# Performance work log

Measured on AMD Instinct MI355X. Metric: run time of the kernel, lower is better.

Reference implementation:

```python
import jax, jax.numpy as jnp
import numpy as np

N = 65536      # total nodes (cells) in batch
E = 262144     # edges per edge type
T = 3          # edge types: row, col, diag
D = 128        # hidden_dim
HG = 4         # gat_heads
DHG = D // HG  # 32, GAT head dim
HH = 4         # hgt_heads
DHH = D // HH  # 32, HGT head dim
B = 32         # boards per batch
SLOPE = 0.2
EPS = 1e-6


def setup_inputs():
    ks = jax.random.split(jax.random.key(0), 32)
    def nrm(i, shape, s=0.05):
        return (jax.random.normal(ks[i], shape) * s).astype(jnp.float32)
    inp = {
        'x_cell': nrm(0, (N, D), 1.0),
        'z_h': nrm(1, (B, D), 1.0),
        'x_cell_embedded': nrm(2, (N, D), 1.0),
        'edge_index': jax.random.randint(ks[3], (T, 2, E), 0, N, dtype=jnp.int32),
        'batch_size': B,
        # GAT conv 1 (one GATConv per edge type, summed)
        'gat1_W': nrm(4, (T, D, D), 0.09),
        'gat1_asrc': nrm(5, (T, HG, DHG), 0.12),
        'gat1_adst': nrm(6, (T, HG, DHG), 0.12),
        'gat1_b': jnp.zeros((T, D), jnp.float32),
        # GAT conv 2
        'gat2_W': nrm(7, (T, D, D), 0.09),
        'gat2_asrc': nrm(8, (T, HG, DHG), 0.12),
        'gat2_adst': nrm(9, (T, HG, DHG), 0.12),
        'gat2_b': jnp.zeros((T, D), jnp.float32),
        # RMSNorms
        'norm1_s': jnp.ones((D,), jnp.float32),
        'norm2_s': jnp.ones((D,), jnp.float32),
        'norm3_s': jnp.ones((D,), jnp.float32),
        # HGT (single node type 'cell', T edge types)
        'hgt_Wk': nrm(10, (D, D), 0.09), 'hgt_bk': jnp.zeros((D,), jnp.float32),
        'hgt_Wq': nrm(11, (D, D), 0.09), 'hgt_bq': jnp.zeros((D,), jnp.float32),
        'hgt_Wv': nrm(12, (D, D), 0.09), 'hgt_bv': jnp.zeros((D,), jnp.float32),
        'hgt_arel': nrm(13, (T, HH, DHH, DHH), 0.15),
        'hgt_mrel': nrm(14, (T, HH, DHH, DHH), 0.15),
        'hgt_prel': jnp.ones((T, HH), jnp.float32),
        'hgt_Wo': nrm(15, (D, D), 0.09), 'hgt_bo': jnp.zeros((D,), jnp.float32),
        'hgt_skip': jnp.ones((), jnp.float32),
        # input injection
        'inj_W': nrm(16, (D, D), 0.09), 'inj_b': jnp.zeros((D,), jnp.float32),
        # FiLM
        'film_W1': nrm(17, (D, 2 * D), 0.09), 'film_b1': jnp.zeros((2 * D,), jnp.float32),
        'film_W2': nrm(18, (2 * D, 2 * D), 0.001), 'film_b2': jnp.zeros((2 * D,), jnp.float32),
    }
    return inp


def _rmsnorm(x, scale):
    return scale * x * jax.lax.rsqrt(jnp.mean(x * x, axis=-1, keepdims=True) + EPS)


def _res(x_old, x_new, scale):
    return jax.nn.leaky_relu(x_old + _rmsnorm(x_new, scale), SLOPE)


def _gat_sum(x, W, asrc, adst, b, src, dst):
    """HeteroConv(sum) over T GATConvs (concat heads, add_self_loops)."""
    loop = jnp.arange(N, dtype=src.dtype)
    def one(Wt, a_s, a_d, bt, s, t):
        s = jnp.concatenate([s, loop])   # self loops
        t = jnp.concatenate([t, loop])
        h = (x @ Wt).reshape(N, HG, DHG)             # [N,H,Dh]
        alpha_src = (h * a_s).sum(-1)                # [N,H]
        alpha_dst = (h * a_d).sum(-1)
        e = jax.nn.leaky_relu(alpha_src[s] + alpha_dst[t], SLOPE)  # [E+N,H]
        m = jax.ops.segment_max(e, t, num_segments=N)
        ex = jnp.exp(e - m[t])
        denom = jax.ops.segment_sum(ex, t, num_segments=N)
        alpha = ex / (denom[t] + 1e-16)
        out = jax.ops.segment_sum(alpha[:, :, None] * h[s], t, num_segments=N)
        return out.reshape(N, D) + bt
    return jax.vmap(one)(W, asrc, adst, b, src, dst).sum(0)


def _hgt(x, Wk, bk, Wq, bq, Wv, bv, a_rel, m_rel, p_rel, Wo, bo, skip, src, dst):
    k = (x @ Wk + bk).reshape(N, HH, DHH)
    q = (x @ Wq + bq).reshape(N, HH, DHH)
    v = (x @ Wv + bv).reshape(N, HH, DHH)
    # per-edge-type relation transforms at node level, then gather per edge
    k_t = jnp.einsum('nhd,thdf->tnhf', k, a_rel)    # [T,N,H,Dk]
    v_t = jnp.einsum('nhd,thdf->tnhf', v, m_rel)
    k_e = jax.vmap(lambda a, i: a[i])(k_t, src)     # [T,E,H,Dk]
    v_e = jax.vmap(lambda a, i: a[i])(v_t, src)
    score = (q[dst] * k_e).sum(-1) * p_rel[:, None, :] / np.sqrt(DHH)  # [T,E,H]
    score = score.reshape(T * E, HH)
    dst_f = dst.reshape(-1)
    m = jax.ops.segment_max(score, dst_f, num_segments=N)
    ex = jnp.exp(score - m[dst_f])
    denom = jax.ops.segment_sum(ex, dst_f, num_segments=N)
    alpha = ex / (denom[dst_f] + 1e-16)
    agg = jax.ops.segment_sum(alpha[:, :, None] * v_e.reshape(T * E, HH, DHH),
                              dst_f, num_segments=N)          # [N,H,Dk]
    out = jax.nn.gelu(agg.reshape(N, D), approximate=False) @ Wo + bo
    sig = jax.nn.sigmoid(skip)
    return sig * out + (1.0 - sig) * x


def _film(nodes, z_h, W1, b1, W2, b2, bsz):
    gb = jax.nn.gelu(z_h @ W1 + b1, approximate=False) @ W2 + b2  # [B,2D]
    gamma, beta = jnp.split(gb, 2, axis=-1)
    gamma = 0.1 * jnp.tanh(gamma)
    beta = 0.1 * jnp.tanh(beta)
    c = N // bsz
    out = (1.0 + gamma)[:, None, :] * nodes.reshape(bsz, c, D) + beta[:, None, :]
    return out.reshape(N, D)


def reference(x_cell, z_h, x_cell_embedded,
              gat1_W, gat1_asrc, gat1_adst, gat1_b,
              gat2_W, gat2_asrc, gat2_adst, gat2_b,
              norm1_s, norm2_s, norm3_s,
              hgt_Wk, hgt_bk, hgt_Wq, hgt_bq, hgt_Wv, hgt_bv,
              hgt_arel, hgt_mrel, hgt_prel, hgt_Wo, hgt_bo, hgt_skip,
              inj_W, inj_b, film_W1, film_b1, film_W2, film_b2,
              edge_index, batch_size):
    src = edge_index[:, 0]
    dst = edge_index[:, 1]
    x1 = _res(x_cell, _gat_sum(x_cell, gat1_W, gat1_asrc, gat1_adst, gat1_b, src, dst), norm1_s)
    x2 = _res(x1, _gat_sum(x1, gat2_W, gat2_asrc, gat2_adst, gat2_b, src, dst), norm2_s)
    x3 = _res(x2, _hgt(x2, hgt_Wk, hgt_bk, hgt_Wq, hgt_bq, hgt_Wv, hgt_bv,
                       hgt_arel, hgt_mrel, hgt_prel, hgt_Wo, hgt_bo, hgt_skip,
                       src, dst), norm3_s)
    x3 = x3 + x_cell_embedded @ inj_W + inj_b
    return _film(x3, z_h, film_W1, film_b1, film_W2, film_b2, batch_size)
```

## Files before the change

### kernel.cpp

```cpp
#include <hip/hip_runtime.h>

#define NN 65536
#define EE 262144
#define ND ((size_t)NN * 128)
#define TBW 132

typedef unsigned short u16;
typedef short bf8_t __attribute__((ext_vector_type(8)));
typedef float f32x4 __attribute__((ext_vector_type(4)));

__device__ __forceinline__ float lrelu(float x){ return x > 0.f ? x : 0.2f*x; }
__device__ __forceinline__ float gelu_exact(float x){ return 0.5f*x*(1.f+erff(x*0.70710678118654752f)); }
__device__ __forceinline__ u16 f2bf(float f){
    union { float f; unsigned u; } v; v.f = f;
    unsigned u = v.u;
    return (u16)((u + 0x7FFFu + ((u >> 16) & 1u)) >> 16);
}
__device__ __forceinline__ float bf2f(u16 b){
    union { unsigned u; float f; } v; v.u = ((unsigned)b) << 16; return v.f;
}
__device__ __forceinline__ float2 bf2x(unsigned p){
    union { unsigned u; float f; } a, b;
    a.u = (p & 0xFFFFu) << 16; b.u = p & 0xFFFF0000u;
    return make_float2(a.f, b.f);
}
__device__ __forceinline__ unsigned cvt2(float a, float b){
    unsigned r; asm("v_cvt_pk_bf16_f32 %0, %1, %2" : "=v"(r) : "v"(a), "v"(b)); return r;
}

__device__ __forceinline__ void load_af32(const float* __restrict__ X, int row, int lk, bf8_t* af){
    #pragma unroll
    for (int kk = 0; kk < 4; ++kk){
        const float* p = X + (size_t)row*128 + kk*32 + lk*8;
        float4 a = *(const float4*)p;
        float4 b = *(const float4*)(p+4);
        union { bf8_t v; unsigned u[4]; } r;
        r.u[0] = cvt2(a.x, a.y); r.u[1] = cvt2(a.z, a.w);
        r.u[2] = cvt2(b.x, b.y); r.u[3] = cvt2(b.z, b.w);
        af[kk] = r.v;
    }
}
__device__ __forceinline__ void load_af16(const u16* __restrict__ X, int row, int lk, bf8_t* af){
    #pragma unroll
    for (int kk = 0; kk < 4; ++kk)
        af[kk] = *(const bf8_t*)(X + (size_t)row*128 + kk*32 + lk*8);
}
__device__ __forceinline__ void mfma_w1(const bf8_t* af, const u16* __restrict__ Wp,
                                        int lr, int lk, f32x4* acc){
    #pragma unroll
    for (int i = 0; i < 8; ++i) acc[i] = (f32x4){0.f,0.f,0.f,0.f};
    #pragma unroll
    for (int kk = 0; kk < 4; ++kk){
        bf8_t B[8];
        #pragma unroll
        for (int nt = 0; nt < 8; ++nt)
            B[nt] = *(const bf8_t*)&Wp[(nt*16+lr)*128 + kk*32 + lk*8];
        #pragma unroll
        for (int nt = 0; nt < 8; ++nt)
            acc[nt] = __builtin_amdgcn_mfma_f32_16x16x32_bf16(af[kk], B[nt], acc[nt], 0, 0, 0);
    }
}
__device__ __forceinline__ void mfma_w2(const bf8_t* af0, const bf8_t* af1,
                                        const u16* __restrict__ Wp,
                                        int lr, int lk, f32x4* acc0, f32x4* acc1){
    #pragma unroll
    for (int i = 0; i < 8; ++i){ acc0[i] = (f32x4){0.f,0.f,0.f,0.f}; acc1[i] = (f32x4){0.f,0.f,0.f,0.f}; }
    #pragma unroll
    for (int kk = 0; kk < 4; ++kk){
        bf8_t B[8];
        #pragma unroll
        for (int nt = 0; nt < 8; ++nt)
            B[nt] = *(const bf8_t*)&Wp[(nt*16+lr)*128 + kk*32 + lk*8];
        #pragma unroll
        for (int nt = 0; nt < 8; ++nt){
            acc0[nt] = __builtin_amdgcn_mfma_f32_16x16x32_bf16(af0[kk], B[nt], acc0[nt], 0, 0, 0);
            acc1[nt] = __builtin_amdgcn_mfma_f32_16x16x32_bf16(af1[kk], B[nt], acc1[nt], 0, 0, 0);
        }
    }
}
__device__ __forceinline__ void acc_to_tb(u16 (*tbw)[TBW], const f32x4* acc, int lr, int lk, const float* bias){
    asm volatile("s_waitcnt lgkmcnt(0)" ::: "memory");
    #pragma unroll
    for (int nt = 0; nt < 8; ++nt){
        int col = nt*16 + lr;
        float badd = bias ? bias[col] : 0.f;
        #pragma unroll
        for (int i = 0; i < 4; ++i) tbw[lk*4+i][col] = f2bf(acc[nt][i] + badd);
    }
    asm volatile("s_waitcnt lgkmcnt(0)" ::: "memory");
}
__device__ __forceinline__ void tb_store(const u16 (*tbw)[TBW], u16* __restrict__ O, int rowbase, int lr, int lk){
    #pragma unroll
    for (int c = 0; c < 4; ++c){
        bf8_t v = *(const bf8_t*)&tbw[c*4+lk][lr*8];
        *(bf8_t*)(O + (size_t)(rowbase + c*4 + lk)*128 + lr*8) = v;
    }
}
__device__ __forceinline__ void tb_frags(const u16 (*tbw)[TBW], int lr, int lk, bf8_t* ha){
    #pragma unroll
    for (int kk = 0; kk < 4; ++kk) ha[kk] = *(const bf8_t*)&tbw[lr][kk*32 + lk*8];
}

__global__ __launch_bounds__(256) void wpack_k(
    const float* __restrict__ g1W, const float* __restrict__ g2W,
    const float* __restrict__ Wk, const float* __restrict__ Wq, const float* __restrict__ Wv,
    const float* __restrict__ Wo, const float* __restrict__ injW,
    const float* __restrict__ arel, const float* __restrict__ mrel,
    const float* __restrict__ g1as, const float* __restrict__ g1ad,
    const float* __restrict__ g2as, const float* __restrict__ g2ad,
    u16* __restrict__ wp, u16* __restrict__ wpa)
{
    int b = blockIdx.x, tid = threadIdx.x;
    if (b < 17) {
        const float* src; int rel = 0;
        if (b < 3) src = g1W + b*16384;
        else if (b < 6) src = g2W + (b-3)*16384;
        else if (b == 6) src = Wk;
        else if (b == 7) src = Wq;
        else if (b == 8) src = Wv;
        else if (b == 9) src = Wo;
        else if (b == 10) src = injW;
        else if (b < 14) { src = arel + (b-11)*4096; rel = 1; }
        else { src = mrel + (b-14)*4096; rel = 1; }
        u16* dst = wp + (size_t)b*16384;
        for (int idx = tid; idx < 16384; idx += 256) {
            int n = idx >> 7, k = idx & 127;
            float v;
            if (rel) v = ((n>>5)==(k>>5)) ? src[(n>>5)*1024 + (k&31)*32 + (n&31)] : 0.f;
            else v = src[k*128 + n];
            dst[idx] = f2bf(v);
        }
    } else {
        for (int idx = tid; idx < 6*2048; idx += 256) {
            int m = idx >> 11;
            int j = idx & 2047;
            int cg = j >> 7, k = j & 127;
            const float* as = (m < 3) ? g1as : g2as;
            const float* ad = (m < 3) ? g1ad : g2ad;
            int t = (m < 3) ? m : m - 3;
            float v = 0.f;
            if (cg < 4)      { if ((k>>5)==cg)   v = as[t*128 + cg*32 + (k&31)]; }
            else if (cg < 8) { int g = cg-4; if ((k>>5)==g) v = ad[t*128 + g*32 + (k&31)]; }
            wpa[idx] = f2bf(v);
        }
    }
}

__global__ __launch_bounds__(256, 2) void gat_gemm3_k(const float* __restrict__ X,
    const u16* __restrict__ wpg, const u16* __restrict__ wpa,
    u16* __restrict__ hb, float* __restrict__ alsb, float* __restrict__ aldb)
{
    __shared__ u16 tb[4][16][TBW];
    const int tid = threadIdx.x, wave = tid>>6, lane = tid&63, lr = lane&15, lk = lane>>4;
    const int rw0 = blockIdx.x*128 + wave*32;
    bf8_t af0[4], af1[4];
    load_af32(X, rw0 + lr, lk, af0);
    load_af32(X, rw0 + 16 + lr, lk, af1);
    f32x4 acc0[8], acc1[8];
    for (int t = 0; t < 3; ++t) {
        mfma_w2(af0, af1, wpg + t*16384, lr, lk, acc0, acc1);
        bf8_t Ba[4];
        #pragma unroll
        for (int kk = 0; kk < 4; ++kk)
            Ba[kk] = *(const bf8_t*)&wpa[t*2048 + lr*128 + kk*32 + lk*8];
        u16* h = hb + (size_t)t*ND;
        float* alst = alsb + (size_t)t*NN*4;
        float* aldt = aldb + (size_t)t*NN*4;
        {
            acc_to_tb(tb[wave], acc0, lr, lk, nullptr);
            tb_store(tb[wave], h, rw0, lr, lk);
            bf8_t ha[4]; tb_frags(tb[wave], lr, lk, ha);
            f32x4 a2 = (f32x4){0.f,0.f,0.f,0.f};
            #pragma unroll
            for (int kk = 0; kk < 4; ++kk)
                a2 = __builtin_amdgcn_mfma_f32_16x16x32_bf16(ha[kk], Ba[kk], a2, 0, 0, 0);
            if (lr < 8){
                float* dp = (lr < 4) ? alst : aldt;
                int g = lr & 3;
                #pragma unroll
                for (int i = 0; i < 4; ++i) dp[(size_t)(rw0 + lk*4 + i)*4 + g] = a2[i];
            }
        }
        {
            acc_to_tb(tb[wave], acc1, lr, lk, nullptr);
            tb_store(tb[wave], h, rw0 + 16, lr, lk);
            bf8_t ha[4]; tb_frags(tb[wave], lr, lk, ha);
            f32x4 a2 = (f32x4){0.f,0.f,0.f,0.f};
            #pragma unroll
            for (int kk = 0; kk < 4; ++kk)
                a2 = __builtin_amdgcn_mfma_f32_16x16x32_bf16(ha[kk], Ba[kk], a2, 0, 0, 0);
            if (lr < 8){
                float* dp = (lr < 4) ? alst : aldt;
                int g = lr & 3;
                #pragma unroll
                for (int i = 0; i < 4; ++i) dp[(size_t)(rw0 + 16 + lk*4 + i)*4 + g] = a2[i];
            }
        }
    }
}

__global__ __launch_bounds__(256, 2) void hgt_proj_k(const float* __restrict__ X,
    const u16* __restrict__ wpk, const u16* __restrict__ wpq, const u16* __restrict__ wpv,
    const u16* __restrict__ wparel, const u16* __restrict__ wpmrel,
    const float* __restrict__ bk, const float* __restrict__ bq, const float* __restrict__ bv,
    u16* __restrict__ qb, u16* __restrict__ ktb, u16* __restrict__ vtb)
{
    __shared__ u16 tb[4][16][TBW];
    const int tid = threadIdx.x, wave = tid>>6, lane = tid&63, lr = lane&15, lk = lane>>4;
    const int rw0 = blockIdx.x*128 + wave*32;
    bf8_t af0[4], af1[4];
    load_af32(X, rw0 + lr, lk, af0);
    load_af32(X, rw0 + 16 + lr, lk, af1);
    f32x4 acc0[8], acc1[8];
    bf8_t ha0[4], ha1[4];
    mfma_w2(af0, af1, wpk, lr, lk, acc0, acc1);
    acc_to_tb(tb[wave], acc0, lr, lk, bk); tb_frags(tb[wave], lr, lk, ha0);
    acc_to_tb(tb[wave], acc1, lr, lk, bk); tb_frags(tb[wave], lr, lk, ha1);
    for (int t = 0; t < 3; ++t){
        mfma_w2(ha0, ha1, wparel + t*16384, lr, lk, acc0, acc1);
        u16* o = ktb + (size_t)t*ND;
        acc_to_tb(tb[wave], acc0, lr, lk, nullptr); tb_store(tb[wave], o, rw0, lr, lk);
        acc_to_tb(tb[wave], acc1, lr, lk, nullptr); tb_store(tb[wave], o, rw0 + 16, lr, lk);
    }
    mfma_w2(af0, af1, wpq, lr, lk, acc0, acc1);
    acc_to_tb(tb[wave], acc0, lr, lk, bq); tb_store(tb[wave], qb, rw0, lr, lk);
    acc_to_tb(tb[wave], acc1, lr, lk, bq); tb_store(tb[wave], qb, rw0 + 16, lr, lk);
    mfma_w2(af0, af1, wpv, lr, lk, acc0, acc1);
    acc_to_tb(tb[wave], acc0, lr, lk, bv); tb_frags(tb[wave], lr, lk, ha0);
    acc_to_tb(tb[wave], acc1, lr, lk, bv); tb_frags(tb[wave], lr, lk, ha1);
    for (int t = 0; t < 3; ++t){
        mfma_w2(ha0, ha1, wpmrel + t*16384, lr, lk, acc0, acc1);
        u16* o = vtb + (size_t)t*ND;
        acc_to_tb(tb[wave], acc0, lr, lk, nullptr); tb_store(tb[wave], o, rw0, lr, lk);
        acc_to_tb(tb[wave], acc1, lr, lk, nullptr); tb_store(tb[wave], o, rw0 + 16, lr, lk);
    }
}

__global__ __launch_bounds__(256) void final_k(const u16* __restrict__ aggb,
    const u16* __restrict__ wpo, const float* __restrict__ bo,
    const float* __restrict__ x2, const float* __restrict__ skipp, const float* __restrict__ scale,
    const float* __restrict__ xemb, const u16* __restrict__ wpinj, const float* __restrict__ injb,
    const float* __restrict__ gbuf, const int* __restrict__ bszp,
    float* __restrict__ out)
{
    const int tid = threadIdx.x, wave = tid>>6, lane = tid&63, lr = lane&15, lk = lane>>4;
    const int rw = blockIdx.x*64 + wave*16;
    bf8_t afa[4]; load_af16(aggb, rw + lr, lk, afa);
    f32x4 acc[8]; mfma_w1(afa, wpo, lr, lk, acc);
    const float sig = 1.f/(1.f + expf(-skipp[0]));
    float vv[8][4], xv[8][4], ss[4] = {0.f,0.f,0.f,0.f};
    #pragma unroll
    for (int nt = 0; nt < 8; ++nt){
        int col = nt*16 + lr;
        float badd = bo[col];
        #pragma unroll
        for (int i = 0; i < 4; ++i){
            float h = acc[nt][i] + badd;
            float x = x2[(size_t)(rw + lk*4 + i)*128 + col];
            float v = sig*h + (1.f - sig)*x;
            vv[nt][i] = v; xv[nt][i] = x;
            ss[i] += v*v;
        }
    }
    #pragma unroll
    for (int i = 0; i < 4; ++i){
        #pragma unroll
        for (int o = 1; o < 16; o <<= 1) ss[i] += __shfl_xor(ss[i], o);
    }
    float rr[4];
    #pragma unroll
    for (int i = 0; i < 4; ++i) rr[i] = rsqrtf(ss[i]*(1.f/128.f) + 1e-6f);
    #pragma unroll
    for (int nt = 0; nt < 8; ++nt){
        int col = nt*16 + lr;
        float sc = scale[col];
        #pragma unroll
        for (int i = 0; i < 4; ++i)
            vv[nt][i] = lrelu(xv[nt][i] + sc*vv[nt][i]*rr[i]);
    }
    bf8_t af2[4]; load_af32(xemb, rw + lr, lk, af2);
    f32x4 acc2[8]; mfma_w1(af2, wpinj, lr, lk, acc2);
    const int cpb = NN / *bszp;
    #pragma unroll
    for (int i = 0; i < 4; ++i){
        int row = rw + lk*4 + i;
        const float* gr = gbuf + (row / cpb)*256;
        #pragma unroll
        for (int nt = 0; nt < 8; ++nt){
            int col = nt*16 + lr;
            float h = vv[nt][i] + acc2[nt][i] + injb[col];
            out[(size_t)row*128 + col] = (1.f + gr[col])*h + gr[128 + col];
        }
    }
}

__global__ __launch_bounds__(256) void hist_k(const int* __restrict__ ei, int* __restrict__ cnt){
    int gid = blockIdx.x*256 + threadIdx.x;
    int t = gid / EE, e = gid - t*EE;
    int d = ei[t*2*EE + EE + e];
    atomicAdd(&cnt[t*NN + d], 1);
}
__global__ __launch_bounds__(256) void scan1_k(const int* __restrict__ cnt, int* __restrict__ off, int* __restrict__ parts){
    __shared__ int sums[256];
    int b = blockIdx.x; int t = b >> 6; int base = (b & 63) * 1024;
    int tid = threadIdx.x;
    int v[4]; int tsum = 0;
    int gbase = t*NN + base + tid*4;
    #pragma unroll
    for (int i = 0; i < 4; ++i){ v[i] = cnt[gbase+i]; tsum += v[i]; }
    sums[tid] = tsum; __syncthreads();
    for (int ofs = 1; ofs < 256; ofs <<= 1) {
        int a = (tid >= ofs) ? sums[tid-ofs] : 0;
        __syncthreads();
        sums[tid] += a;
        __syncthreads();
    }
    int run = sums[tid] - tsum;
    int obase = t*(NN+1) + base + tid*4;
    #pragma unroll
    for (int i = 0; i < 4; ++i){ off[obase+i] = run; run += v[i]; }
    if (tid == 255) parts[b] = sums[255];
}
__global__ void scan2_k(int* parts){
    if (threadIdx.x == 0 && blockIdx.x == 0) {
        for (int t = 0; t < 3; ++t) {
            int run = 0;
            for (int i = 0; i < 64; ++i) { int b = t*64+i; int v = parts[b]; parts[b] = run; run += v; }
        }
    }
}
__global__ __launch_bounds__(256) void scan3_k(int* __restrict__ off, const int* __restrict__ parts){
    int b = blockIdx.x; int t = b >> 6; int base = (b & 63) * 1024;
    int add = parts[b];
    int idx = t*(NN+1) + base + threadIdx.x*4;
    #pragma unroll
    for (int i = 0; i < 4; ++i) off[idx+i] += add;
    if (threadIdx.x == 0 && (b & 63) == 0) off[t*(NN+1) + NN] = EE;
}
__global__ __launch_bounds__(256) void scatter_k(const int* __restrict__ ei, const int* __restrict__ off,
                                                 int* __restrict__ cur, int* __restrict__ out){
    int gid = blockIdx.x*256 + threadIdx.x;
    int t = gid / EE, e = gid - t*EE;
    int s = ei[t*2*EE + e];
    int d = ei[t*2*EE + EE + e];
    int p = atomicAdd(&cur[t*NN + d], 1);
    out[t*EE + off[t*(NN+1)+d] + p] = s;
}

__global__ __launch_bounds__(256) void gat_aggres_k(const u16* __restrict__ hb,
    const float* __restrict__ alsb, const float* __restrict__ aldb,
    const int* __restrict__ coff, const int* __restrict__ csrc,
    const float* __restrict__ bias3, const float* __restrict__ xold,
    const float* __restrict__ scale, float* __restrict__ out)
{
    int gid = blockIdx.x*256 + threadIdx.x;
    int node = gid >> 6, lane = gid & 63;
    int g = lane >> 4;
    float a0 = 0.f, a1 = 0.f;
    for (int t = 0; t < 3; ++t) {
        const u16* h = hb + (size_t)t*ND;
        const float* als = alsb + (size_t)t*NN*4;
        float ad = aldb[(size_t)t*NN*4 + node*4 + g];
        float aself = als[node*4 + g];
        int beg = coff[t*(NN+1) + node], end = coff[t*(NN+1) + node + 1];
        float ex = expf(lrelu(aself + ad));
        float dsum = ex;
        float2 hv = bf2x(*(const unsigned*)&h[(size_t)node*128 + lane*2]);
        float s0 = ex*hv.x, s1 = ex*hv.y;
        for (int e = beg; e < end; ++e) {
            int s = csrc[t*EE + e];
            float exx = expf(lrelu(als[s*4 + g] + ad));
            float2 hw = bf2x(*(const unsigned*)&h[(size_t)s*128 + lane*2]);
            dsum += exx; s0 += exx*hw.x; s1 += exx*hw.y;
        }
        float inv = 1.f/(dsum + 1e-16f);
        a0 += s0*inv; a1 += s1*inv;
    }
    int c0 = lane*2;
    a0 += bias3[c0]   + bias3[128+c0]   + bias3[256+c0];
    a1 += bias3[c0+1] + bias3[128+c0+1] + bias3[256+c0+1];
    float ssum = a0*a0 + a1*a1;
    #pragma unroll
    for (int o = 1; o < 64; o <<= 1) ssum += __shfl_xor(ssum, o);
    float r = rsqrtf(ssum*(1.f/128.f) + 1e-6f);
    size_t off = (size_t)node*128 + c0;
    float2 xo = *(const float2*)&xold[off];
    out[off]   = lrelu(xo.x + scale[c0]*a0*r);
    out[off+1] = lrelu(xo.y + scale[c0+1]*a1*r);
}

__global__ __launch_bounds__(256) void hgt_agg_k(const u16* __restrict__ ktb,
    const u16* __restrict__ vtb, const u16* __restrict__ qb,
    const float* __restrict__ prel, const int* __restrict__ coff,
    const int* __restrict__ csrc, u16* __restrict__ aggb)
{
    int gid = blockIdx.x*256 + threadIdx.x;
    int node = gid >> 6, lane = gid & 63;
    int hh = lane >> 4;
    float2 qv = bf2x(*(const unsigned*)&qb[(size_t)node*128 + lane*2]);
    float dsum = 0.f, a0 = 0.f, a1 = 0.f;
    for (int t = 0; t < 3; ++t) {
        float ph = prel[t*4 + hh] * 0.17677669529663689f;
        int beg = coff[t*(NN+1) + node], end = coff[t*(NN+1) + node + 1];
        const u16* kt = ktb + (size_t)t*ND;
        const u16* vt = vtb + (size_t)t*ND;
        for (int e = beg; e < end; ++e) {
            int s = csrc[t*EE + e];
            size_t ro = (size_t)s*128 + lane*2;
            float2 kv = bf2x(*(const unsigned*)&kt[ro]);
            float sc = qv.x*kv.x + qv.y*kv.y;
            #pragma unroll
            for (int o = 1; o < 16; o <<= 1) sc += __shfl_xor(sc, o);
            float ex = expf(sc * ph);
            float2 vx = bf2x(*(const unsigned*)&vt[ro]);
            dsum += ex; a0 += ex*vx.x; a1 += ex*vx.y;
        }
    }
    float inv = 1.f/(dsum + 1e-16f);
    size_t o = (size_t)node*128 + lane*2;
    aggb[o]   = f2bf(gelu_exact(a0*inv));
    aggb[o+1] = f2bf(gelu_exact(a1*inv));
}

__global__ __launch_bounds__(256) void film_k(const float* __restrict__ z,
    const float* __restrict__ W1, const float* __restrict__ b1,
    const float* __restrict__ W2, const float* __restrict__ b2,
    float* __restrict__ gb)
{
    __shared__ float zr[128];
    __shared__ float g1[256];
    int r = blockIdx.x, tid = threadIdx.x;
    if (tid < 128) zr[tid] = z[r*128 + tid];
    __syncthreads();
    float s = b1[tid];
    for (int k = 0; k < 128; ++k) s += zr[k]*W1[k*256 + tid];
    g1[tid] = gelu_exact(s);
    __syncthreads();
    float s2 = b2[tid];
    for (int k = 0; k < 256; ++k) s2 += g1[k]*W2[k*256 + tid];
    gb[r*256 + tid] = 0.1f*tanhf(s2);
}

extern "C" void kernel_launch(void* const* d_in, const int* in_sizes, int n_in,
                              void* d_out, int out_size, void* d_ws, size_t ws_size,
                              hipStream_t stream)
{
    const float* x_cell = (const float*)d_in[0];
    const float* z_h    = (const float*)d_in[1];
    const float* x_emb  = (const float*)d_in[2];
    const int*   eidx   = (const int*)d_in[3];
    const int*   bszp   = (const int*)d_in[4];
    const float* g1W  = (const float*)d_in[5];
    const float* g1as = (const float*)d_in[6];
    const float* g1ad = (const float*)d_in[7];
    const float* g1b  = (const float*)d_in[8];
    const float* g2W  = (const float*)d_in[9];
    const float* g2as = (const float*)d_in[10];
    const float* g2ad = (const float*)d_in[11];
    const float* g2b  = (const float*)d_in[12];
    const float* n1s  = (const float*)d_in[13];
    const float* n2s  = (const float*)d_in[14];
    const float* n3s  = (const float*)d_in[15];
    const float* Wk   = (const float*)d_in[16];
    const float* bk   = (const float*)d_in[17];
    const float* Wq   = (const float*)d_in[18];
    const float* bq   = (const float*)d_in[19];
    const float* Wv   = (const float*)d_in[20];
    const float* bv   = (const float*)d_in[21];
    const float* arel = (const float*)d_in[22];
    const float* mrel = (const float*)d_in[23];
    const float* prel = (const float*)d_in[24];
    const float* Wo   = (const float*)d_in[25];
    const float* bo   = (const float*)d_in[26];
    const float* skipp= (const float*)d_in[27];
    const float* injW = (const float*)d_in[28];
    const float* injb = (const float*)d_in[29];
    const float* fW1  = (const float*)d_in[30];
    const float* fb1  = (const float*)d_in[31];
    const float* fW2  = (const float*)d_in[32];
    const float* fb2  = (const float*)d_in[33];

    u16* wp   = (u16*)d_ws;
    u16* wpa  = wp + (size_t)17*16384;
    float* x2   = (float*)(wpa + 6*2048);
    float* alsb = x2 + ND;
    float* aldb = alsb + (size_t)3*NN*4;
    float* gbuf = aldb + (size_t)3*NN*4;
    int* coff   = (int*)(gbuf + 32*256);
    int* csrc   = coff + 3*(NN+1);
    int* tmpc   = csrc + 3*EE;
    int* parts  = tmpc + 3*NN;
    u16* R1     = (u16*)(parts + 256);
    u16* R2     = R1 + 3*ND;

    u16* hb  = R1;
    u16* qb  = R1 + ND;
    u16* ktb = R2;
    u16* vtb = R2 + 3*ND;
    u16* aggb = R1;
    float* x1   = (float*)d_out;
    float* outp = (float*)d_out;

    const u16* wpg1 = wp;
    const u16* wpg2 = wp + (size_t)3*16384;
    const u16* wpk  = wp + (size_t)6*16384;
    const u16* wpq  = wp + (size_t)7*16384;
    const u16* wpv  = wp + (size_t)8*16384;
    const u16* wpo  = wp + (size_t)9*16384;
    const u16* wpinj= wp + (size_t)10*16384;
    const u16* wparel = wp + (size_t)11*16384;
    const u16* wpmrel = wp + (size_t)14*16384;

    wpack_k<<<18, 256, 0, stream>>>(g1W, g2W, Wk, Wq, Wv, Wo, injW, arel, mrel,
                                    g1as, g1ad, g2as, g2ad, wp, wpa);

    hipMemsetAsync(tmpc, 0, 3*NN*sizeof(int), stream);
    hist_k<<<3*EE/256, 256, 0, stream>>>(eidx, tmpc);
    scan1_k<<<192, 256, 0, stream>>>(tmpc, coff, parts);
    scan2_k<<<1, 64, 0, stream>>>(parts);
    scan3_k<<<192, 256, 0, stream>>>(coff, parts);
    hipMemsetAsync(tmpc, 0, 3*NN*sizeof(int), stream);
    scatter_k<<<3*EE/256, 256, 0, stream>>>(eidx, coff, tmpc, csrc);

    int B = in_sizes[1] / 128;
    film_k<<<B, 256, 0, stream>>>(z_h, fW1, fb1, fW2, fb2, gbuf);

    gat_gemm3_k<<<512, 256, 0, stream>>>(x_cell, wpg1, wpa, hb, alsb, aldb);
    gat_aggres_k<<<16384, 256, 0, stream>>>(hb, alsb, aldb, coff, csrc, g1b, x_cell, n1s, x1);

    gat_gemm3_k<<<512, 256, 0, stream>>>(x1, wpg2, wpa + 3*2048, hb, alsb, aldb);
    gat_aggres_k<<<16384, 256, 0, stream>>>(hb, alsb, aldb, coff, csrc, g2b, x1, n2s, x2);

    hgt_proj_k<<<512, 256, 0, stream>>>(x2, wpk, wpq, wpv, wparel, wpmrel,
                                        bk, bq, bv, qb, ktb, vtb);
    hgt_agg_k<<<16384, 256, 0, stream>>>(ktb, vtb, qb, prel, coff, csrc, aggb);

    final_k<<<1024, 256, 0, stream>>>(aggb, wpo, bo, x2, skipp, n3s,
                                      x_emb, wpinj, injb, gbuf, bszp, outp);
}
```

Baseline: 666.2 us.

## Fold HGT relation matrices into query and post-aggregation, store intermediates in bf16

The HGT key relation transform is moved onto the query side (q·A_rel^T) and the message relation transform is applied after per-type aggregation inside the final kernel. Gathered K and V are therefore plain shared projections interleaved per node, so the edge loop reads one 256-wide row instead of per-type K/V tensors. Intermediate activations x1 and x2 are now kept in bf16, which halves their read/write traffic. In exchange the final kernel does three extra GEMMs, and storing residual states in bf16 adds rounding error.

```diff
diff --git a/kernel.cpp b/kernel.cpp
--- a/kernel.cpp
+++ b/kernel.cpp
@@ -45,20 +45,24 @@
     for (int kk = 0; kk < 4; ++kk)
         af[kk] = *(const bf8_t*)(X + (size_t)row*128 + kk*32 + lk*8);
 }
+__device__ __forceinline__ void mfma_w1_acc(const bf8_t* af, const u16* __restrict__ Wp,
+                                            int lr, int lk, f32x4* acc){
+    #pragma unroll
+    for (int kk = 0; kk < 4; ++kk){
+        bf8_t B[8];
+        #pragma unroll
+        for (int nt = 0; nt < 8; ++nt)
+            B[nt] = *(const bf8_t*)&Wp[(nt*16+lr)*128 + kk*32 + lk*8];
+        #pragma unroll
+        for (int nt = 0; nt < 8; ++nt)
+            acc[nt] = __builtin_amdgcn_mfma_f32_16x16x32_bf16(af[kk], B[nt], acc[nt], 0, 0, 0);
+    }
+}
 __device__ __forceinline__ void mfma_w1(const bf8_t* af, const u16* __restrict__ Wp,
                                         int lr, int lk, f32x4* acc){
     #pragma unroll
     for (int i = 0; i < 8; ++i) acc[i] = (f32x4){0.f,0.f,0.f,0.f};
-    #pragma unroll
-    for (int kk = 0; kk < 4; ++kk){
-        bf8_t B[8];
-        #pragma unroll
-        for (int nt = 0; nt < 8; ++nt)
-            B[nt] = *(const bf8_t*)&Wp[(nt*16+lr)*128 + kk*32 + lk*8];
-        #pragma unroll
-        for (int nt = 0; nt < 8; ++nt)
-            acc[nt] = __builtin_amdgcn_mfma_f32_16x16x32_bf16(af[kk], B[nt], acc[nt], 0, 0, 0);
-    }
+    mfma_w1_acc(af, Wp, lr, lk, acc);
 }
 __device__ __forceinline__ void mfma_w2(const bf8_t* af0, const bf8_t* af1,
                                         const u16* __restrict__ Wp,
@@ -89,11 +93,21 @@
     }
     asm volatile("s_waitcnt lgkmcnt(0)" ::: "memory");
 }
-__device__ __forceinline__ void tb_store(const u16 (*tbw)[TBW], u16* __restrict__ O, int rowbase, int lr, int lk){
+__device__ __forceinline__ void acc_to_tb_gelu(u16 (*tbw)[TBW], const f32x4* acc, int lr, int lk){
+    asm volatile("s_waitcnt lgkmcnt(0)" ::: "memory");
+    #pragma unroll
+    for (int nt = 0; nt < 8; ++nt){
+        int col = nt*16 + lr;
+        #pragma unroll
+        for (int i = 0; i < 4; ++i) tbw[lk*4+i][col] = f2bf(gelu_exact(acc[nt][i]));
+    }
+    asm volatile("s_waitcnt lgkmcnt(0)" ::: "memory");
+}
+__device__ __forceinline__ void tb_store(const u16 (*tbw)[TBW], u16* __restrict__ O, size_t rowstride, int rowbase, int lr, int lk){
     #pragma unroll
     for (int c = 0; c < 4; ++c){
         bf8_t v = *(const bf8_t*)&tbw[c*4+lk][lr*8];
-        *(bf8_t*)(O + (size_t)(rowbase + c*4 + lk)*128 + lr*8) = v;
+        *(bf8_t*)(O + (size_t)(rowbase + c*4 + lk)*rowstride + lr*8) = v;
     }
 }
 __device__ __forceinline__ void tb_frags(const u16 (*tbw)[TBW], int lr, int lk, bf8_t* ha){
@@ -120,14 +134,15 @@
         else if (b == 8) src = Wv;
         else if (b == 9) src = Wo;
         else if (b == 10) src = injW;
-        else if (b < 14) { src = arel + (b-11)*4096; rel = 1; }
+        else if (b < 14) { src = arel + (b-11)*4096; rel = 2; }
         else { src = mrel + (b-14)*4096; rel = 1; }
         u16* dst = wp + (size_t)b*16384;
         for (int idx = tid; idx < 16384; idx += 256) {
             int n = idx >> 7, k = idx & 127;
             float v;
-            if (rel) v = ((n>>5)==(k>>5)) ? src[(n>>5)*1024 + (k&31)*32 + (n&31)] : 0.f;
-            else v = src[k*128 + n];
+            if (rel == 1)      v = ((n>>5)==(k>>5)) ? src[(n>>5)*1024 + (k&31)*32 + (n&31)] : 0.f;
+            else if (rel == 2) v = ((n>>5)==(k>>5)) ? src[(n>>5)*1024 + (n&31)*32 + (k&31)] : 0.f;
+            else               v = src[k*128 + n];
             dst[idx] = f2bf(v);
         }
     } else {
@@ -146,7 +161,8 @@
     }
 }
 
-__global__ __launch_bounds__(256, 2) void gat_gemm3_k(const float* __restrict__ X,
+template<int AF32>
+__global__ __launch_bounds__(256, 2) void gat_gemm3_k(const float* __restrict__ Xf, const u16* __restrict__ Xb,
     const u16* __restrict__ wpg, const u16* __restrict__ wpa,
     u16* __restrict__ hb, float* __restrict__ alsb, float* __restrict__ aldb)
 {
@@ -154,8 +170,8 @@
     const int tid = threadIdx.x, wave = tid>>6, lane = tid&63, lr = lane&15, lk = lane>>4;
     const int rw0 = blockIdx.x*128 + wave*32;
     bf8_t af0[4], af1[4];
-    load_af32(X, rw0 + lr, lk, af0);
-    load_af32(X, rw0 + 16 + lr, lk, af1);
+    if (AF32){ load_af32(Xf, rw0 + lr, lk, af0); load_af32(Xf, rw0 + 16 + lr, lk, af1); }
+    else     { load_af16(Xb, rw0 + lr, lk, af0); load_af16(Xb, rw0 + 16 + lr, lk, af1); }
     f32x4 acc0[8], acc1[8];
     for (int t = 0; t < 3; ++t) {
         mfma_w2(af0, af1, wpg + t*16384, lr, lk, acc0, acc1);
@@ -168,7 +184,7 @@
         float* aldt = aldb + (size_t)t*NN*4;
         {
             acc_to_tb(tb[wave], acc0, lr, lk, nullptr);
-            tb_store(tb[wave], h, rw0, lr, lk);
+            tb_store(tb[wave], h, 128, rw0, lr, lk);
             bf8_t ha[4]; tb_frags(tb[wave], lr, lk, ha);
             f32x4 a2 = (f32x4){0.f,0.f,0.f,0.f};
             #pragma unroll
@@ -183,7 +199,7 @@
         }
         {
             acc_to_tb(tb[wave], acc1, lr, lk, nullptr);
-            tb_store(tb[wave], h, rw0 + 16, lr, lk);
+            tb_store(tb[wave], h, 128, rw0 + 16, lr, lk);
             bf8_t ha[4]; tb_frags(tb[wave], lr, lk, ha);
             f32x4 a2 = (f32x4){0.f,0.f,0.f,0.f};
             #pragma unroll
@@ -199,54 +215,92 @@
     }
 }
 
-__global__ __launch_bounds__(256, 2) void hgt_proj_k(const float* __restrict__ X,
+__global__ __launch_bounds__(256, 2) void hgt_proj_k(const u16* __restrict__ X,
     const u16* __restrict__ wpk, const u16* __restrict__ wpq, const u16* __restrict__ wpv,
-    const u16* __restrict__ wparel, const u16* __restrict__ wpmrel,
+    const u16* __restrict__ wparel,
     const float* __restrict__ bk, const float* __restrict__ bq, const float* __restrict__ bv,
-    u16* __restrict__ qb, u16* __restrict__ ktb, u16* __restrict__ vtb)
+    u16* __restrict__ kvb, u16* __restrict__ qtb)
 {
     __shared__ u16 tb[4][16][TBW];
     const int tid = threadIdx.x, wave = tid>>6, lane = tid&63, lr = lane&15, lk = lane>>4;
     const int rw0 = blockIdx.x*128 + wave*32;
     bf8_t af0[4], af1[4];
-    load_af32(X, rw0 + lr, lk, af0);
-    load_af32(X, rw0 + 16 + lr, lk, af1);
+    load_af16(X, rw0 + lr, lk, af0);
+    load_af16(X, rw0 + 16 + lr, lk, af1);
     f32x4 acc0[8], acc1[8];
+    mfma_w2(af0, af1, wpk, lr, lk, acc0, acc1);
+    acc_to_tb(tb[wave], acc0, lr, lk, bk); tb_store(tb[wave], kvb, 256, rw0, lr, lk);
+    acc_to_tb(tb[wave], acc1, lr, lk, bk); tb_store(tb[wave], kvb, 256, rw0 + 16, lr, lk);
+    mfma_w2(af0, af1, wpv, lr, lk, acc0, acc1);
+    acc_to_tb(tb[wave], acc0, lr, lk, bv); tb_store(tb[wave], kvb + 128, 256, rw0, lr, lk);
+    acc_to_tb(tb[wave], acc1, lr, lk, bv); tb_store(tb[wave], kvb + 128, 256, rw0 + 16, lr, lk);
     bf8_t ha0[4], ha1[4];
-    mfma_w2(af0, af1, wpk, lr, lk, acc0, acc1);
-    acc_to_tb(tb[wave], acc0, lr, lk, bk); tb_frags(tb[wave], lr, lk, ha0);
-    acc_to_tb(tb[wave], acc1, lr, lk, bk); tb_frags(tb[wave], lr, lk, ha1);
+    mfma_w2(af0, af1, wpq, lr, lk, acc0, acc1);
+    acc_to_tb(tb[wave], acc0, lr, lk, bq); tb_frags(tb[wave], lr, lk, ha0);
+    acc_to_tb(tb[wave], acc1, lr, lk, bq); tb_frags(tb[wave], lr, lk, ha1);
     for (int t = 0; t < 3; ++t){
         mfma_w2(ha0, ha1, wparel + t*16384, lr, lk, acc0, acc1);
-        u16* o = ktb + (size_t)t*ND;
-        acc_to_tb(tb[wave], acc0, lr, lk, nullptr); tb_store(tb[wave], o, rw0, lr, lk);
-        acc_to_tb(tb[wave], acc1, lr, lk, nullptr); tb_store(tb[wave], o, rw0 + 16, lr, lk);
-    }
-    mfma_w2(af0, af1, wpq, lr, lk, acc0, acc1);
-    acc_to_tb(tb[wave], acc0, lr, lk, bq); tb_store(tb[wave], qb, rw0, lr, lk);
-    acc_to_tb(tb[wave], acc1, lr, lk, bq); tb_store(tb[wave], qb, rw0 + 16, lr, lk);
-    mfma_w2(af0, af1, wpv, lr, lk, acc0, acc1);
-    acc_to_tb(tb[wave], acc0, lr, lk, bv); tb_frags(tb[wave], lr, lk, ha0);
-    acc_to_tb(tb[wave], acc1, lr, lk, bv); tb_frags(tb[wave], lr, lk, ha1);
-    for (int t = 0; t < 3; ++t){
-        mfma_w2(ha0, ha1, wpmrel + t*16384, lr, lk, acc0, acc1);
-        u16* o = vtb + (size_t)t*ND;
-        acc_to_tb(tb[wave], acc0, lr, lk, nullptr); tb_store(tb[wave], o, rw0, lr, lk);
-        acc_to_tb(tb[wave], acc1, lr, lk, nullptr); tb_store(tb[wave], o, rw0 + 16, lr, lk);
-    }
-}
-
-__global__ __launch_bounds__(256) void final_k(const u16* __restrict__ aggb,
-    const u16* __restrict__ wpo, const float* __restrict__ bo,
-    const float* __restrict__ x2, const float* __restrict__ skipp, const float* __restrict__ scale,
+        u16* o = qtb + (size_t)t*ND;
+        acc_to_tb(tb[wave], acc0, lr, lk, nullptr); tb_store(tb[wave], o, 128, rw0, lr, lk);
+        acc_to_tb(tb[wave], acc1, lr, lk, nullptr); tb_store(tb[wave], o, 128, rw0 + 16, lr, lk);
+    }
+}
+
+__global__ __launch_bounds__(256) void hgt_agg_k(const u16* __restrict__ kvb,
+    const u16* __restrict__ qtb, const float* __restrict__ prel,
+    const int* __restrict__ coff, const int* __restrict__ csrc,
+    u16* __restrict__ pb)
+{
+    int gid = blockIdx.x*256 + threadIdx.x;
+    int node = gid >> 6, lane = gid & 63;
+    int hh = lane >> 4;
+    float a0[3], a1[3];
+    float dsum = 0.f;
+    #pragma unroll
+    for (int t = 0; t < 3; ++t) {
+        a0[t] = 0.f; a1[t] = 0.f;
+        float ph = prel[t*4 + hh] * 0.17677669529663689f;
+        float2 qv = bf2x(*(const unsigned*)&qtb[(size_t)t*ND + (size_t)node*128 + lane*2]);
+        int beg = coff[t*(NN+1) + node], end = coff[t*(NN+1) + node + 1];
+        for (int e = beg; e < end; ++e) {
+            int s = csrc[t*EE + e];
+            size_t ro = (size_t)s*256 + lane*2;
+            float2 kv = bf2x(*(const unsigned*)&kvb[ro]);
+            float sc = qv.x*kv.x + qv.y*kv.y;
+            #pragma unroll
+            for (int o = 1; o < 16; o <<= 1) sc += __shfl_xor(sc, o);
+            float ex = expf(sc * ph);
+            float2 vx = bf2x(*(const unsigned*)&kvb[ro + 128]);
+            dsum += ex; a0[t] += ex*vx.x; a1[t] += ex*vx.y;
+        }
+    }
+    float inv = 1.f/(dsum + 1e-16f);
+    size_t o = (size_t)node*128 + lane*2;
+    #pragma unroll
+    for (int t = 0; t < 3; ++t)
+        *(unsigned*)&pb[(size_t)t*ND + o] = cvt2(a0[t]*inv, a1[t]*inv);
+}
+
+__global__ __launch_bounds__(256) void final_k(const u16* __restrict__ pb,
+    const u16* __restrict__ wpmrel, const u16* __restrict__ wpo, const float* __restrict__ bo,
+    const u16* __restrict__ x2b, const float* __restrict__ skipp, const float* __restrict__ scale,
     const float* __restrict__ xemb, const u16* __restrict__ wpinj, const float* __restrict__ injb,
     const float* __restrict__ gbuf, const int* __restrict__ bszp,
     float* __restrict__ out)
 {
+    __shared__ u16 tb[4][16][TBW];
     const int tid = threadIdx.x, wave = tid>>6, lane = tid&63, lr = lane&15, lk = lane>>4;
     const int rw = blockIdx.x*64 + wave*16;
-    bf8_t afa[4]; load_af16(aggb, rw + lr, lk, afa);
-    f32x4 acc[8]; mfma_w1(afa, wpo, lr, lk, acc);
+    f32x4 acc[8];
+    #pragma unroll
+    for (int i = 0; i < 8; ++i) acc[i] = (f32x4){0.f,0.f,0.f,0.f};
+    for (int t = 0; t < 3; ++t){
+        bf8_t af[4]; load_af16(pb + (size_t)t*ND, rw + lr, lk, af);
+        mfma_w1_acc(af, wpmrel + t*16384, lr, lk, acc);
+    }
+    acc_to_tb_gelu(tb[wave], acc, lr, lk);
+    bf8_t ga[4]; tb_frags(tb[wave], lr, lk, ga);
+    mfma_w1(ga, wpo, lr, lk, acc);
     const float sig = 1.f/(1.f + expf(-skipp[0]));
     float vv[8][4], xv[8][4], ss[4] = {0.f,0.f,0.f,0.f};
     #pragma unroll
@@ -256,7 +310,7 @@
         #pragma unroll
         for (int i = 0; i < 4; ++i){
             float h = acc[nt][i] + badd;
-            float x = x2[(size_t)(rw + lk*4 + i)*128 + col];
+            float x = bf2f(x2b[(size_t)(rw + lk*4 + i)*128 + col]);
             float v = sig*h + (1.f - sig)*x;
             vv[nt][i] = v; xv[nt][i] = x;
             ss[i] += v*v;
@@ -347,11 +401,12 @@
     out[t*EE + off[t*(NN+1)+d] + p] = s;
 }
 
+template<int XF32>
 __global__ __launch_bounds__(256) void gat_aggres_k(const u16* __restrict__ hb,
     const float* __restrict__ alsb, const float* __restrict__ aldb,
     const int* __restrict__ coff, const int* __restrict__ csrc,
-    const float* __restrict__ bias3, const float* __restrict__ xold,
-    const float* __restrict__ scale, float* __restrict__ out)
+    const float* __restrict__ bias3, const float* __restrict__ xoldf, const u16* __restrict__ xoldb,
+    const float* __restrict__ scale, u16* __restrict__ outb)
 {
     int gid = blockIdx.x*256 + threadIdx.x;
     int node = gid >> 6, lane = gid & 63;
@@ -384,42 +439,12 @@
     for (int o = 1; o < 64; o <<= 1) ssum += __shfl_xor(ssum, o);
     float r = rsqrtf(ssum*(1.f/128.f) + 1e-6f);
     size_t off = (size_t)node*128 + c0;
-    float2 xo = *(const float2*)&xold[off];
-    out[off]   = lrelu(xo.x + scale[c0]*a0*r);
-    out[off+1] = lrelu(xo.y + scale[c0+1]*a1*r);
-}
-
-__global__ __launch_bounds__(256) void hgt_agg_k(const u16* __restrict__ ktb,
-    const u16* __restrict__ vtb, const u16* __restrict__ qb,
-    const float* __restrict__ prel, const int* __restrict__ coff,
-    const int* __restrict__ csrc, u16* __restrict__ aggb)
-{
-    int gid = blockIdx.x*256 + threadIdx.x;
-    int node = gid >> 6, lane = gid & 63;
-    int hh = lane >> 4;
-    float2 qv = bf2x(*(const unsigned*)&qb[(size_t)node*128 + lane*2]);
-    float dsum = 0.f, a0 = 0.f, a1 = 0.f;
-    for (int t = 0; t < 3; ++t) {
-        float ph = prel[t*4 + hh] * 0.17677669529663689f;
-        int beg = coff[t*(NN+1) + node], end = coff[t*(NN+1) + node + 1];
-        const u16* kt = ktb + (size_t)t*ND;
-        const u16* vt = vtb + (size_t)t*ND;
-        for (int e = beg; e < end; ++e) {
-            int s = csrc[t*EE + e];
-            size_t ro = (size_t)s*128 + lane*2;
-            float2 kv = bf2x(*(const unsigned*)&kt[ro]);
-            float sc = qv.x*kv.x + qv.y*kv.y;
-            #pragma unroll
-            for (int o = 1; o < 16; o <<= 1) sc += __shfl_xor(sc, o);
-            float ex = expf(sc * ph);
-            float2 vx = bf2x(*(const unsigned*)&vt[ro]);
-            dsum += ex; a0 += ex*vx.x; a1 += ex*vx.y;
-        }
-    }
-    float inv = 1.f/(dsum + 1e-16f);
-    size_t o = (size_t)node*128 + lane*2;
-    aggb[o]   = f2bf(gelu_exact(a0*inv));
-    aggb[o+1] = f2bf(gelu_exact(a1*inv));
+    float2 xo;
+    if (XF32) xo = *(const float2*)&xoldf[off];
+    else      xo = bf2x(*(const unsigned*)&xoldb[off]);
+    float y0 = lrelu(xo.x + scale[c0]*a0*r);
+    float y1 = lrelu(xo.y + scale[c0+1]*a1*r);
+    *(unsigned*)&outb[off] = cvt2(y0, y1);
 }
 
 __global__ __launch_bounds__(256) void film_k(const float* __restrict__ z,
@@ -482,23 +507,20 @@
 
     u16* wp   = (u16*)d_ws;
     u16* wpa  = wp + (size_t)17*16384;
-    float* x2   = (float*)(wpa + 6*2048);
-    float* alsb = x2 + ND;
+    u16* x1b  = wpa + 6*2048;
+    u16* x2b  = x1b + ND;
+    u16* kvb  = x2b + ND;
+    u16* pb   = kvb + 2*ND;
+    u16* hb   = pb + 3*ND;
+    float* alsb = (float*)(hb + 3*ND);
     float* aldb = alsb + (size_t)3*NN*4;
     float* gbuf = aldb + (size_t)3*NN*4;
     int* coff   = (int*)(gbuf + 32*256);
     int* csrc   = coff + 3*(NN+1);
     int* tmpc   = csrc + 3*EE;
     int* parts  = tmpc + 3*NN;
-    u16* R1     = (u16*)(parts + 256);
-    u16* R2     = R1 + 3*ND;
-
-    u16* hb  = R1;
-    u16* qb  = R1 + ND;
-    u16* ktb = R2;
-    u16* vtb = R2 + 3*ND;
-    u16* aggb = R1;
-    float* x1   = (float*)d_out;
+
+    u16* qtb = hb;
     float* outp = (float*)d_out;
 
     const u16* wpg1 = wp;
@@ -525,16 +547,16 @@
     int B = in_sizes[1] / 128;
     film_k<<<B, 256, 0, stream>>>(z_h, fW1, fb1, fW2, fb2, gbuf);
 
-    gat_gemm3_k<<<512, 256, 0, stream>>>(x_cell, wpg1, wpa, hb, alsb, aldb);
-    gat_aggres_k<<<16384, 256, 0, stream>>>(hb, alsb, aldb, coff, csrc, g1b, x_cell, n1s, x1);
-
-    gat_gemm3_k<<<512, 256, 0, stream>>>(x1, wpg2, wpa + 3*2048, hb, alsb, aldb);
-    gat_aggres_k<<<16384, 256, 0, stream>>>(hb, alsb, aldb, coff, csrc, g2b, x1, n2s, x2);
-
-    hgt_proj_k<<<512, 256, 0, stream>>>(x2, wpk, wpq, wpv, wparel, wpmrel,
-                                        bk, bq, bv, qb, ktb, vtb);
-    hgt_agg_k<<<16384, 256, 0, stream>>>(ktb, vtb, qb, prel, coff, csrc, aggb);
-
-    final_k<<<1024, 256, 0, stream>>>(aggb, wpo, bo, x2, skipp, n3s,
+    gat_gemm3_k<1><<<512, 256, 0, stream>>>(x_cell, nullptr, wpg1, wpa, hb, alsb, aldb);
+    gat_aggres_k<1><<<16384, 256, 0, stream>>>(hb, alsb, aldb, coff, csrc, g1b, x_cell, nullptr, n1s, x1b);
+
+    gat_gemm3_k<0><<<512, 256, 0, stream>>>(nullptr, x1b, wpg2, wpa + 3*2048, hb, alsb, aldb);
+    gat_aggres_k<0><<<16384, 256, 0, stream>>>(hb, alsb, aldb, coff, csrc, g2b, nullptr, x1b, n2s, x2b);
+
+    hgt_proj_k<<<512, 256, 0, stream>>>(x2b, wpk, wpq, wpv, wparel,
+                                        bk, bq, bv, kvb, qtb);
+    hgt_agg_k<<<16384, 256, 0, stream>>>(kvb, qtb, prel, coff, csrc, pb);
+
+    final_k<<<1024, 256, 0, stream>>>(pb, wpmrel, wpo, bo, x2b, skipp, n3s,
                                       x_emb, wpinj, injb, gbuf, bszp, outp);
 }
```

Measured after the change: 694.7 us. +4.3%, slower.
